# Optimization experiments

Measured on AMD Instinct MI355X. Metric: run time of the kernel, lower is better.

The kernel has to match this reference:

```python
import jax, jax.numpy as jnp
import numpy as np

B, S, H = 1, 2048, 2048
NH, NKV, HD = 16, 4, 128
LAT, RD = 512, 64
ND = HD - RD  # nope_dim = 64
EPS = 1e-6


def _rms(x, g):
    return x * jax.lax.rsqrt(jnp.mean(x * x, axis=-1, keepdims=True) + EPS) * g


def _rotate_half(x):
    x1, x2 = jnp.split(x, 2, axis=-1)
    return jnp.concatenate([-x2, x1], axis=-1)


def _rope(x, cos, sin):
    # x: [B,S,nh,RD]; cos/sin: [S,RD] -> broadcast over batch and heads
    c = cos[None, :, None, :]
    s = sin[None, :, None, :]
    return x * c + _rotate_half(x) * s


def setup_inputs() -> dict:
    key = jax.random.key(0)
    ks = jax.random.split(key, 10)
    x = jax.random.normal(ks[0], (B, S, H), jnp.float32)
    # rotary tables (theta=10000) for rope_dim
    inv = 1.0 / (10000.0 ** (np.arange(0, RD, 2, dtype=np.float32) / RD))
    t = np.arange(S, dtype=np.float32)
    freqs = np.outer(t, inv)  # [S, RD/2]
    emb = np.concatenate([freqs, freqs], axis=-1)  # [S, RD]
    cos = jnp.asarray(np.cos(emb), jnp.float32)
    sin = jnp.asarray(np.sin(emb), jnp.float32)
    sc = lambda fan_in: 1.0 / np.sqrt(fan_in)
    Wq_nope = jax.random.normal(ks[1], (NH * ND, H), jnp.float32) * sc(H)
    Wq_rope = jax.random.normal(ks[2], (NH * RD, H), jnp.float32) * sc(H)
    W_kv_down = jax.random.normal(ks[3], (LAT, H), jnp.float32) * sc(H)
    W_k_nope = jax.random.normal(ks[4], (NKV * ND, LAT), jnp.float32) * sc(LAT)
    W_k_rope = jax.random.normal(ks[5], (NKV * RD, LAT), jnp.float32) * sc(LAT)
    W_v = jax.random.normal(ks[6], (NKV * HD, LAT), jnp.float32) * sc(LAT)
    W_o = jax.random.normal(ks[7], (H, NH * HD), jnp.float32) * sc(NH * HD)
    return {
        "x": x, "cos": cos, "sin": sin,
        "Wq_nope": Wq_nope, "Wq_rope": Wq_rope,
        "g_qnope": jnp.ones((ND,), jnp.float32),
        "g_qrope": jnp.ones((RD,), jnp.float32),
        "W_kv_down": W_kv_down, "g_ckv": jnp.ones((LAT,), jnp.float32),
        "W_k_nope": W_k_nope, "W_k_rope": W_k_rope,
        "W_v": W_v, "W_o": W_o,
    }


def reference(x, cos, sin, Wq_nope, Wq_rope, g_qnope, g_qrope,
              W_kv_down, g_ckv, W_k_nope, W_k_rope, W_v, W_o):
    n_rep = NH // NKV
    # queries: decoupled nope / rope parts, RMSNorm each, RoPE on rope part
    q_nope = _rms((x @ Wq_nope.T).reshape(B, S, NH, ND), g_qnope)
    q_rope = _rms((x @ Wq_rope.T).reshape(B, S, NH, RD), g_qrope)
    q_rope = _rope(q_rope, cos[:S, :RD], sin[:S, :RD])
    q = jnp.concatenate([q_nope, q_rope], axis=-1)  # [B,S,NH,HD]
    # latent KV compression
    c_kv = _rms(x @ W_kv_down.T, g_ckv)  # [B,S,LAT]
    k_nope = (c_kv @ W_k_nope.T).reshape(B, S, NKV, ND)
    k_rope = _rope((c_kv @ W_k_rope.T).reshape(B, S, NKV, RD), cos[:S, :RD], sin[:S, :RD])
    v = (c_kv @ W_v.T).reshape(B, S, NKV, HD)
    k = jnp.concatenate([k_nope, k_rope], axis=-1)  # [B,S,NKV,HD]
    # repeat kv heads
    k = jnp.repeat(k, n_rep, axis=2)  # [B,S,NH,HD]
    v = jnp.repeat(v, n_rep, axis=2)
    # causal attention, softmax in fp32
    scores = jnp.einsum("bqhd,bkhd->bhqk", q, k) / jnp.sqrt(jnp.asarray(HD, jnp.float32))
    causal = jnp.tril(jnp.ones((S, S), bool))
    scores = jnp.where(causal[None, None], scores, -jnp.inf)
    attn = jax.nn.softmax(scores.astype(jnp.float32), axis=-1).astype(q.dtype)
    out = jnp.einsum("bhqk,bkhd->bqhd", attn, v).reshape(B, S, NH * HD)
    return out @ W_o.T  # [B,S,H]
```

## Files before the change

### kernel.cpp

```cpp
#include <hip/hip_runtime.h>
#include <hip/hip_bf16.h>
#include <math.h>

#define TPB 256

typedef __attribute__((ext_vector_type(8))) short bf16x8;
typedef __attribute__((ext_vector_type(4))) float f32x4;

__device__ __forceinline__ short f2bs(float x) {
  __hip_bfloat16 h = __float2bfloat16(x);
  return *reinterpret_cast<short*>(&h);
}

__device__ __forceinline__ void gll16(const void* g, void* l) {
  __builtin_amdgcn_global_load_lds(
      (const __attribute__((address_space(1))) unsigned int*)g,
      (__attribute__((address_space(3))) unsigned int*)l, 16, 0, 0);
}

__global__ __launch_bounds__(TPB) void cvt_f2b(
    const float* __restrict__ s, short* __restrict__ d, int n)
{
  int i = (blockIdx.x * TPB + threadIdx.x) << 2;
  if (i >= n) return;
  const float4 v = *(const float4*)(s + i);
  short4 o;
  o.x = f2bs(v.x); o.y = f2bs(v.y); o.z = f2bs(v.z); o.w = f2bs(v.w);
  *(short4*)(d + i) = o;
}

__global__ __launch_bounds__(TPB) void cvt_weights(
    const float* __restrict__ w0, const float* __restrict__ w1,
    const float* __restrict__ w2, const float* __restrict__ w3,
    const float* __restrict__ w4, const float* __restrict__ w5,
    const float* __restrict__ w6,
    short* __restrict__ Wcat, short* __restrict__ Wkvb, short* __restrict__ Wob)
{
  int b = blockIdx.x;
  const float* src; short* dst; int base;
  if (b < 2048)      { src = w0; dst = Wcat;           base = b; }
  else if (b < 4096) { src = w1; dst = Wcat + 2097152; base = b - 2048; }
  else if (b < 5120) { src = w2; dst = Wcat + 4194304; base = b - 4096; }
  else if (b < 5248) { src = w3; dst = Wkvb;           base = b - 5120; }
  else if (b < 5376) { src = w4; dst = Wkvb + 131072;  base = b - 5248; }
  else if (b < 5632) { src = w5; dst = Wkvb + 262144;  base = b - 5376; }
  else               { src = w6; dst = Wob;            base = b - 5632; }
  int i = base * 1024 + threadIdx.x * 4;
  float4 v = *(const float4*)(src + i);
  short4 o;
  o.x = f2bs(v.x); o.y = f2bs(v.y); o.z = f2bs(v.z); o.w = f2bs(v.w);
  *(short4*)(dst + i) = o;
}

__global__ __launch_bounds__(TPB) void rms512b(
    const float* __restrict__ src, short* __restrict__ dst,
    const float* __restrict__ g, int nrows)
{
  int row = blockIdx.x * (TPB / 64) + (threadIdx.x >> 6);
  int l = threadIdx.x & 63;
  if (row >= nrows) return;
  const float* p = src + (size_t)row * 512;
  float x[8];
  float ss = 0.f;
#pragma unroll
  for (int i = 0; i < 8; ++i) { x[i] = p[i * 64 + l]; ss += x[i] * x[i]; }
#pragma unroll
  for (int msk = 1; msk < 64; msk <<= 1) ss += __shfl_xor(ss, msk);
  float r = rsqrtf(ss * (1.0f / 512.0f) + 1e-6f);
#pragma unroll
  for (int i = 0; i < 8; ++i)
    dst[(size_t)row * 512 + i * 64 + l] = f2bs(x[i] * r * g[i * 64 + l]);
}

template <int MODE>
__global__ __launch_bounds__(TPB) void gemm_fused(
    const short* __restrict__ A, const short* __restrict__ W,
    float* __restrict__ Cf, short* __restrict__ qk_out, short* __restrict__ vt,
    float* __restrict__ ckv_f,
    const float* __restrict__ cosb, const float* __restrict__ sinb,
    const float* __restrict__ g_qnope, const float* __restrict__ g_qrope,
    int M, int N, int K, int ldc)
{
  __shared__ short As[2][128 * 64];
  __shared__ short Bs[2][128 * 64];
  const int t = threadIdx.x;
  const int lane = t & 63, wave = t >> 6;
  const int wr = wave >> 1, wc = wave & 1;
  const int li = lane & 15, lh = lane >> 4;
  const int bm = blockIdx.y * 128, bn = blockIdx.x * 128;

  f32x4 acc[4][4];
#pragma unroll
  for (int m = 0; m < 4; ++m)
#pragma unroll
    for (int n = 0; n < 4; ++n) acc[m][n] = (f32x4){0.f, 0.f, 0.f, 0.f};

#define GSTAGE(buf, k0)                                                        \
  {                                                                            \
    _Pragma("unroll") for (int i = 0; i < 4; ++i) {                            \
      int id = i * 256 + t;                                                    \
      int r = id >> 3, cl = id & 7;                                            \
      gll16(A + (size_t)(bm + r) * K + (k0) + ((cl ^ (r & 7)) << 3),           \
            &As[buf][id * 8]);                                                 \
    }                                                                          \
    _Pragma("unroll") for (int i = 0; i < 4; ++i) {                            \
      int id = i * 256 + t;                                                    \
      int r = id >> 3, cl = id & 7;                                            \
      gll16(W + (size_t)(bn + r) * K + (k0) + ((cl ^ (r & 7)) << 3),           \
            &Bs[buf][id * 8]);                                                 \
    }                                                                          \
  }

  GSTAGE(0, 0);
  int cur = 0;
  for (int k0 = 0; k0 < K; k0 += 64) {
    __syncthreads();
    if (k0 + 64 < K) GSTAGE(cur ^ 1, k0 + 64);
    bf16x8 af[2][4], bf[2][4];
#pragma unroll
    for (int m = 0; m < 4; ++m) {
      int r = wr * 64 + m * 16 + li;
#pragma unroll
      for (int kd = 0; kd < 2; ++kd)
        af[kd][m] = *(const bf16x8*)&As[cur][r * 64 + (((kd * 4 + lh) ^ (r & 7)) << 3)];
    }
#pragma unroll
    for (int n = 0; n < 4; ++n) {
      int r = wc * 64 + n * 16 + li;
#pragma unroll
      for (int kd = 0; kd < 2; ++kd)
        bf[kd][n] = *(const bf16x8*)&Bs[cur][r * 64 + (((kd * 4 + lh) ^ (r & 7)) << 3)];
    }
#pragma unroll
    for (int kd = 0; kd < 2; ++kd)
#pragma unroll
      for (int m = 0; m < 4; ++m)
#pragma unroll
        for (int n = 0; n < 4; ++n)
          acc[m][n] = __builtin_amdgcn_mfma_f32_16x16x32_bf16(af[kd][m], bf[kd][n],
                                                              acc[m][n], 0, 0, 0);
    cur ^= 1;
  }
#undef GSTAGE

  const int colbase = bn + wc * 64;

  if (MODE == 0) {
#pragma unroll
    for (int m = 0; m < 4; ++m) {
      int gm = bm + wr * 64 + m * 16 + lh * 4;
#pragma unroll
      for (int n = 0; n < 4; ++n) {
        int gn = colbase + n * 16 + li;
#pragma unroll
        for (int j = 0; j < 4; ++j)
          Cf[(size_t)(gm + j) * ldc + gn] = acc[m][n][j];
      }
    }
  }

  if (MODE == 1) {
    if (colbase < 2048) {
      const bool isrope = colbase >= 1024;
      const int head = (colbase & 1023) >> 6;
      const float* g = isrope ? g_qrope : g_qnope;
      float gv[4];
#pragma unroll
      for (int nf = 0; nf < 4; ++nf) gv[nf] = g[nf * 16 + li];
#pragma unroll
      for (int m = 0; m < 4; ++m) {
#pragma unroll
        for (int j = 0; j < 4; ++j) {
          int s = bm + wr * 64 + m * 16 + lh * 4 + j;
          float sum = acc[m][0][j] * acc[m][0][j] + acc[m][1][j] * acc[m][1][j] +
                      acc[m][2][j] * acc[m][2][j] + acc[m][3][j] * acc[m][3][j];
          sum += __shfl_xor(sum, 1); sum += __shfl_xor(sum, 2);
          sum += __shfl_xor(sum, 4); sum += __shfl_xor(sum, 8);
          float r = rsqrtf(sum * (1.0f / 64.0f) + 1e-6f);
          float y[4];
#pragma unroll
          for (int nf = 0; nf < 4; ++nf) y[nf] = acc[m][nf][j] * r * gv[nf];
          if (isrope) {
            float yr[4];
#pragma unroll
            for (int nf = 0; nf < 4; ++nf) {
              int c = nf * 16 + li;
              float cs = cosb[s * 64 + c], sn = sinb[s * 64 + c];
              float par = (nf < 2) ? -y[nf + 2] : y[nf - 2];
              yr[nf] = y[nf] * cs + par * sn;
            }
#pragma unroll
            for (int nf = 0; nf < 4; ++nf) y[nf] = yr[nf];
          }
#pragma unroll
          for (int nf = 0; nf < 4; ++nf)
            qk_out[(size_t)s * 2048 + head * 128 + (isrope ? 64 : 0) + nf * 16 + li] =
                f2bs(y[nf]);
        }
      }
    } else {
      const int c0 = colbase - 2048;
#pragma unroll
      for (int m = 0; m < 4; ++m) {
        int gm = bm + wr * 64 + m * 16 + lh * 4;
#pragma unroll
        for (int n = 0; n < 4; ++n) {
          int c = c0 + n * 16 + li;
#pragma unroll
          for (int j = 0; j < 4; ++j)
            ckv_f[(size_t)(gm + j) * 512 + c] = acc[m][n][j];
        }
      }
    }
  }

  if (MODE == 2) {
    if (colbase < 512) {
      const bool isrope = colbase >= 256;
      const int kvh = (colbase & 255) >> 6;
#pragma unroll
      for (int m = 0; m < 4; ++m) {
#pragma unroll
        for (int j = 0; j < 4; ++j) {
          int s = bm + wr * 64 + m * 16 + lh * 4 + j;
          float y[4];
#pragma unroll
          for (int nf = 0; nf < 4; ++nf) y[nf] = acc[m][nf][j];
          if (isrope) {
            float yr[4];
#pragma unroll
            for (int nf = 0; nf < 4; ++nf) {
              int c = nf * 16 + li;
              float cs = cosb[s * 64 + c], sn = sinb[s * 64 + c];
              float par = (nf < 2) ? -y[nf + 2] : y[nf - 2];
              yr[nf] = y[nf] * cs + par * sn;
            }
#pragma unroll
            for (int nf = 0; nf < 4; ++nf) y[nf] = yr[nf];
          }
#pragma unroll
          for (int nf = 0; nf < 4; ++nf)
            qk_out[(size_t)s * 512 + kvh * 128 + (isrope ? 64 : 0) + nf * 16 + li] =
                f2bs(y[nf]);
        }
      }
    } else {
#pragma unroll
      for (int m = 0; m < 4; ++m) {
        int s0 = bm + wr * 64 + m * 16 + lh * 4;
#pragma unroll
        for (int nf = 0; nf < 4; ++nf) {
          int d = colbase - 512 + nf * 16 + li;
          int kvh = d >> 7, dd = d & 127;
          short4 pk;
          pk.x = f2bs(acc[m][nf][0]); pk.y = f2bs(acc[m][nf][1]);
          pk.z = f2bs(acc[m][nf][2]); pk.w = f2bs(acc[m][nf][3]);
          *(short4*)&vt[(size_t)kvh * 262144 + (size_t)dd * 2048 + s0] = pk;
        }
      }
    }
  }
}

__global__ __launch_bounds__(TPB) void attn_mfma(
    const short* __restrict__ qb, const short* __restrict__ kb,
    const short* __restrict__ vt, short* __restrict__ ob)
{
  __shared__ short Ks[2][64 * 128];
  __shared__ short Vs[2][128 * 64];
  __shared__ short Ps[4][16 * 64];
  const int h = blockIdx.x;
  const int qt = gridDim.y - 1 - blockIdx.y;
  const int kvh = h >> 2;
  const int t = threadIdx.x, lane = t & 63, wave = t >> 6;
  const int li = lane & 15, lh = lane >> 4;
  const int q0 = qt * 64, q0w = q0 + wave * 16;
  const float scale = 0.08838834764831845f;

  bf16x8 qf[4];
#pragma unroll
  for (int kd = 0; kd < 4; ++kd)
    qf[kd] = *(const bf16x8*)(qb + (size_t)(q0w + li) * 2048 + h * 128 + kd * 32 + lh * 8);

  f32x4 o[8];
#pragma unroll
  for (int n = 0; n < 8; ++n) o[n] = (f32x4){0.f, 0.f, 0.f, 0.f};
  float m_i[4] = {-1e30f, -1e30f, -1e30f, -1e30f};
  float l_i[4] = {0.f, 0.f, 0.f, 0.f};

#define ASTAGE(buf, kbase)                                                     \
  {                                                                            \
    _Pragma("unroll") for (int i = 0; i < 4; ++i) {                            \
      int c = t + i * 256;                                                     \
      int kpos = c >> 4, dcl = (c & 15) ^ (kpos & 7);                          \
      gll16(kb + (size_t)((kbase) + kpos) * 512 + kvh * 128 + dcl * 8,         \
            &Ks[buf][c * 8]);                                                  \
    }                                                                          \
    _Pragma("unroll") for (int i = 0; i < 4; ++i) {                            \
      int c = t + i * 256;                                                     \
      int d = c >> 3, kpl = (c & 7) ^ (d & 7);                                 \
      gll16(vt + (size_t)kvh * 262144 + (size_t)d * 2048 + (kbase) + kpl * 8,  \
            &Vs[buf][c * 8]);                                                  \
    }                                                                          \
  }

  short* pw = Ps[wave];
  const int nkt = qt + 1;
  ASTAGE(0, 0);
  int cur = 0;
  for (int kt = 0; kt < nkt; ++kt) {
    const int kbase = kt * 64;
    __syncthreads();
    if (kt + 1 < nkt) ASTAGE(cur ^ 1, kbase + 64);

    f32x4 s[4];
#pragma unroll
    for (int n = 0; n < 4; ++n) s[n] = (f32x4){0.f, 0.f, 0.f, 0.f};
#pragma unroll
    for (int n = 0; n < 4; ++n) {
      int kpos = n * 16 + li;
#pragma unroll
      for (int kd = 0; kd < 4; ++kd) {
        int cph = (kd * 4 + lh) ^ (kpos & 7);
        bf16x8 kf = *(const bf16x8*)&Ks[cur][kpos * 128 + cph * 8];
        s[n] = __builtin_amdgcn_mfma_f32_16x16x32_bf16(qf[kd], kf, s[n], 0, 0, 0);
      }
    }
    float sv[4][4];
    const bool diag = (kt == nkt - 1);
#pragma unroll
    for (int n = 0; n < 4; ++n)
#pragma unroll
      for (int j = 0; j < 4; ++j) {
        float val = s[n][j] * scale;
        if (diag) {
          int kg = kbase + n * 16 + li;
          int qg = q0w + lh * 4 + j;
          if (kg > qg) val = -1e30f;
        }
        sv[n][j] = val;
      }
    float c_[4];
#pragma unroll
    for (int j = 0; j < 4; ++j) {
      float rm = fmaxf(fmaxf(sv[0][j], sv[1][j]), fmaxf(sv[2][j], sv[3][j]));
      rm = fmaxf(rm, __shfl_xor(rm, 1));
      rm = fmaxf(rm, __shfl_xor(rm, 2));
      rm = fmaxf(rm, __shfl_xor(rm, 4));
      rm = fmaxf(rm, __shfl_xor(rm, 8));
      float mn = fmaxf(m_i[j], rm);
      c_[j] = __expf(m_i[j] - mn);
      m_i[j] = mn;
    }
#pragma unroll
    for (int n = 0; n < 4; ++n)
#pragma unroll
      for (int j = 0; j < 4; ++j) sv[n][j] = __expf(sv[n][j] - m_i[j]);
#pragma unroll
    for (int j = 0; j < 4; ++j) {
      float rs = sv[0][j] + sv[1][j] + sv[2][j] + sv[3][j];
      rs += __shfl_xor(rs, 1);
      rs += __shfl_xor(rs, 2);
      rs += __shfl_xor(rs, 4);
      rs += __shfl_xor(rs, 8);
      l_i[j] = l_i[j] * c_[j] + rs;
    }
#pragma unroll
    for (int n = 0; n < 4; ++n)
#pragma unroll
      for (int j = 0; j < 4; ++j) {
        int qq = lh * 4 + j, kp = n * 16 + li;
        pw[qq * 64 + (kp ^ ((qq & 7) << 3))] = f2bs(sv[n][j]);
      }
#pragma unroll
    for (int n = 0; n < 8; ++n)
#pragma unroll
      for (int j = 0; j < 4; ++j) o[n][j] *= c_[j];
    asm volatile("s_waitcnt lgkmcnt(0)" ::: "memory");
    __builtin_amdgcn_sched_barrier(0);
#pragma unroll
    for (int kk = 0; kk < 2; ++kk) {
      int kp0 = kk * 32 + lh * 8;
      bf16x8 pf = *(const bf16x8*)&pw[li * 64 + (kp0 ^ ((li & 7) << 3))];
#pragma unroll
      for (int n = 0; n < 8; ++n) {
        int d = n * 16 + li;
        bf16x8 vf = *(const bf16x8*)&Vs[cur][d * 64 + (kp0 ^ ((d & 7) << 3))];
        o[n] = __builtin_amdgcn_mfma_f32_16x16x32_bf16(pf, vf, o[n], 0, 0, 0);
      }
    }
    cur ^= 1;
  }
#undef ASTAGE
  float inv[4];
#pragma unroll
  for (int j = 0; j < 4; ++j) inv[j] = 1.0f / l_i[j];
#pragma unroll
  for (int n = 0; n < 8; ++n)
#pragma unroll
    for (int j = 0; j < 4; ++j)
      ob[(size_t)(q0w + lh * 4 + j) * 2048 + h * 128 + n * 16 + li] =
          f2bs(o[n][j] * inv[j]);
}

extern "C" void kernel_launch(void* const* d_in, const int* in_sizes, int n_in,
                              void* d_out, int out_size, void* d_ws, size_t ws_size,
                              hipStream_t stream) {
  const float* x         = (const float*)d_in[0];
  const float* cosb      = (const float*)d_in[1];
  const float* sinb      = (const float*)d_in[2];
  const float* Wq_nope   = (const float*)d_in[3];
  const float* Wq_rope   = (const float*)d_in[4];
  const float* g_qnope   = (const float*)d_in[5];
  const float* g_qrope   = (const float*)d_in[6];
  const float* W_kv_down = (const float*)d_in[7];
  const float* g_ckv     = (const float*)d_in[8];
  const float* W_k_nope  = (const float*)d_in[9];
  const float* W_k_rope  = (const float*)d_in[10];
  const float* W_v       = (const float*)d_in[11];
  const float* W_o       = (const float*)d_in[12];
  float* out = (float*)d_out;

  float* ws = (float*)d_ws;
  float* ckv_f = ws;
  short* sb   = (short*)(ws + 1048576);
  short* xb   = sb;
  short* Wcat = sb + 4194304;
  short* Wkvb = Wcat + 5242880;
  short* Wob  = Wkvb + 524288;
  short* qb   = Wob + 4194304;
  short* ckvb = qb + 4194304;
  short* kb   = ckvb + 1048576;
  short* vt   = kb + 1048576;
  short* aob  = xb;

  dim3 blk(TPB);

  cvt_f2b<<<4096, blk, 0, stream>>>(x, xb, 4194304);
  cvt_weights<<<9728, blk, 0, stream>>>(Wq_nope, Wq_rope, W_kv_down, W_k_nope,
                                        W_k_rope, W_v, W_o, Wcat, Wkvb, Wob);

  gemm_fused<1><<<dim3(20, 16), blk, 0, stream>>>(
      xb, Wcat, nullptr, qb, nullptr, ckv_f, cosb, sinb, g_qnope, g_qrope,
      2048, 2560, 2048, 0);

  rms512b<<<512, blk, 0, stream>>>(ckv_f, ckvb, g_ckv, 2048);

  gemm_fused<2><<<dim3(8, 16), blk, 0, stream>>>(
      ckvb, Wkvb, nullptr, kb, vt, nullptr, cosb, sinb, nullptr, nullptr,
      2048, 1024, 512, 0);

  attn_mfma<<<dim3(16, 32), blk, 0, stream>>>(qb, kb, vt, aob);

  gemm_fused<0><<<dim3(16, 16), blk, 0, stream>>>(
      aob, Wob, out, nullptr, nullptr, nullptr, nullptr, nullptr, nullptr, nullptr,
      2048, 2048, 2048, 2048);
}
```

Measured before the change: 286.2 us.

## Load attention K/V directly from global, tighten GEMM pipeline waits, use exp2 softmax

The attention kernel drops its LDS double-buffering of K and V. Each wave now reads its K and V fragments straight from global memory, which removes block-wide barriers and frees LDS for higher occupancy, at the cost of repeated global and L2 traffic across waves. The softmax folds log2(e) into the scale and uses exp2f, and it skips rescaling the output accumulator when no row maximum changed. The GEMM loop replaces __syncthreads with an explicit lgkmcnt wait plus barrier and a partial vmcnt wait so the next stage's loads can stay in flight, and it raises wave priority around the MFMA block.

```diff
diff --git a/kernel.cpp b/kernel.cpp
--- a/kernel.cpp
+++ b/kernel.cpp
@@ -114,8 +114,17 @@
   GSTAGE(0, 0);
   int cur = 0;
   for (int k0 = 0; k0 < K; k0 += 64) {
-    __syncthreads();
-    if (k0 + 64 < K) GSTAGE(cur ^ 1, k0 + 64);
+    __builtin_amdgcn_sched_barrier(0);
+    asm volatile("s_waitcnt lgkmcnt(0)" ::: "memory");
+    __builtin_amdgcn_s_barrier();
+    __builtin_amdgcn_sched_barrier(0);
+    if (k0 + 64 < K) {
+      GSTAGE(cur ^ 1, k0 + 64);
+      asm volatile("s_waitcnt vmcnt(8)" ::: "memory");
+    } else {
+      asm volatile("s_waitcnt vmcnt(0)" ::: "memory");
+    }
+    __builtin_amdgcn_sched_barrier(0);
     bf16x8 af[2][4], bf[2][4];
 #pragma unroll
     for (int m = 0; m < 4; ++m) {
@@ -131,6 +140,7 @@
       for (int kd = 0; kd < 2; ++kd)
         bf[kd][n] = *(const bf16x8*)&Bs[cur][r * 64 + (((kd * 4 + lh) ^ (r & 7)) << 3)];
     }
+    __builtin_amdgcn_s_setprio(1);
 #pragma unroll
     for (int kd = 0; kd < 2; ++kd)
 #pragma unroll
@@ -139,6 +149,8 @@
         for (int n = 0; n < 4; ++n)
           acc[m][n] = __builtin_amdgcn_mfma_f32_16x16x32_bf16(af[kd][m], bf[kd][n],
                                                               acc[m][n], 0, 0, 0);
+    __builtin_amdgcn_s_setprio(0);
+    __builtin_amdgcn_sched_barrier(0);
     cur ^= 1;
   }
 #undef GSTAGE
@@ -266,16 +278,14 @@
     const short* __restrict__ qb, const short* __restrict__ kb,
     const short* __restrict__ vt, short* __restrict__ ob)
 {
-  __shared__ short Ks[2][64 * 128];
-  __shared__ short Vs[2][128 * 64];
   __shared__ short Ps[4][16 * 64];
   const int h = blockIdx.x;
   const int qt = gridDim.y - 1 - blockIdx.y;
   const int kvh = h >> 2;
   const int t = threadIdx.x, lane = t & 63, wave = t >> 6;
   const int li = lane & 15, lh = lane >> 4;
-  const int q0 = qt * 64, q0w = q0 + wave * 16;
-  const float scale = 0.08838834764831845f;
+  const int q0w = qt * 64 + wave * 16;
+  const float sc2 = 0.08838834764831845f * 1.44269504088896f;
 
   bf16x8 qf[4];
 #pragma unroll
@@ -288,52 +298,35 @@
   float m_i[4] = {-1e30f, -1e30f, -1e30f, -1e30f};
   float l_i[4] = {0.f, 0.f, 0.f, 0.f};
 
-#define ASTAGE(buf, kbase)                                                     \
-  {                                                                            \
-    _Pragma("unroll") for (int i = 0; i < 4; ++i) {                            \
-      int c = t + i * 256;                                                     \
-      int kpos = c >> 4, dcl = (c & 15) ^ (kpos & 7);                          \
-      gll16(kb + (size_t)((kbase) + kpos) * 512 + kvh * 128 + dcl * 8,         \
-            &Ks[buf][c * 8]);                                                  \
-    }                                                                          \
-    _Pragma("unroll") for (int i = 0; i < 4; ++i) {                            \
-      int c = t + i * 256;                                                     \
-      int d = c >> 3, kpl = (c & 7) ^ (d & 7);                                 \
-      gll16(vt + (size_t)kvh * 262144 + (size_t)d * 2048 + (kbase) + kpl * 8,  \
-            &Vs[buf][c * 8]);                                                  \
-    }                                                                          \
-  }
-
   short* pw = Ps[wave];
+  const short* kbh = kb + kvh * 128;
+  const short* vth = vt + (size_t)kvh * 262144;
   const int nkt = qt + 1;
-  ASTAGE(0, 0);
-  int cur = 0;
+
   for (int kt = 0; kt < nkt; ++kt) {
     const int kbase = kt * 64;
-    __syncthreads();
-    if (kt + 1 < nkt) ASTAGE(cur ^ 1, kbase + 64);
-
     f32x4 s[4];
 #pragma unroll
     for (int n = 0; n < 4; ++n) s[n] = (f32x4){0.f, 0.f, 0.f, 0.f};
 #pragma unroll
-    for (int n = 0; n < 4; ++n) {
-      int kpos = n * 16 + li;
-#pragma unroll
-      for (int kd = 0; kd < 4; ++kd) {
-        int cph = (kd * 4 + lh) ^ (kpos & 7);
-        bf16x8 kf = *(const bf16x8*)&Ks[cur][kpos * 128 + cph * 8];
-        s[n] = __builtin_amdgcn_mfma_f32_16x16x32_bf16(qf[kd], kf, s[n], 0, 0, 0);
-      }
+    for (int kd = 0; kd < 4; ++kd) {
+      bf16x8 kf[4];
+#pragma unroll
+      for (int n = 0; n < 4; ++n)
+        kf[n] = *(const bf16x8*)(kbh + (size_t)(kbase + n * 16 + li) * 512 +
+                                 kd * 32 + lh * 8);
+#pragma unroll
+      for (int n = 0; n < 4; ++n)
+        s[n] = __builtin_amdgcn_mfma_f32_16x16x32_bf16(qf[kd], kf[n], s[n], 0, 0, 0);
     }
     float sv[4][4];
-    const bool diag = (kt == nkt - 1);
+    const bool dg = (kt == nkt - 1);
 #pragma unroll
     for (int n = 0; n < 4; ++n)
 #pragma unroll
       for (int j = 0; j < 4; ++j) {
-        float val = s[n][j] * scale;
-        if (diag) {
+        float val = s[n][j] * sc2;
+        if (dg) {
           int kg = kbase + n * 16 + li;
           int qg = q0w + lh * 4 + j;
           if (kg > qg) val = -1e30f;
@@ -341,6 +334,7 @@
         sv[n][j] = val;
       }
     float c_[4];
+    float cmin = 1.f;
 #pragma unroll
     for (int j = 0; j < 4; ++j) {
       float rm = fmaxf(fmaxf(sv[0][j], sv[1][j]), fmaxf(sv[2][j], sv[3][j]));
@@ -349,13 +343,14 @@
       rm = fmaxf(rm, __shfl_xor(rm, 4));
       rm = fmaxf(rm, __shfl_xor(rm, 8));
       float mn = fmaxf(m_i[j], rm);
-      c_[j] = __expf(m_i[j] - mn);
+      c_[j] = exp2f(m_i[j] - mn);
       m_i[j] = mn;
+      cmin = fminf(cmin, c_[j]);
     }
 #pragma unroll
     for (int n = 0; n < 4; ++n)
 #pragma unroll
-      for (int j = 0; j < 4; ++j) sv[n][j] = __expf(sv[n][j] - m_i[j]);
+      for (int j = 0; j < 4; ++j) sv[n][j] = exp2f(sv[n][j] - m_i[j]);
 #pragma unroll
     for (int j = 0; j < 4; ++j) {
       float rs = sv[0][j] + sv[1][j] + sv[2][j] + sv[3][j];
@@ -372,10 +367,12 @@
         int qq = lh * 4 + j, kp = n * 16 + li;
         pw[qq * 64 + (kp ^ ((qq & 7) << 3))] = f2bs(sv[n][j]);
       }
-#pragma unroll
-    for (int n = 0; n < 8; ++n)
-#pragma unroll
-      for (int j = 0; j < 4; ++j) o[n][j] *= c_[j];
+    if (__any(cmin < 1.f)) {
+#pragma unroll
+      for (int n = 0; n < 8; ++n)
+#pragma unroll
+        for (int j = 0; j < 4; ++j) o[n][j] *= c_[j];
+    }
     asm volatile("s_waitcnt lgkmcnt(0)" ::: "memory");
     __builtin_amdgcn_sched_barrier(0);
 #pragma unroll
@@ -384,14 +381,11 @@
       bf16x8 pf = *(const bf16x8*)&pw[li * 64 + (kp0 ^ ((li & 7) << 3))];
 #pragma unroll
       for (int n = 0; n < 8; ++n) {
-        int d = n * 16 + li;
-        bf16x8 vf = *(const bf16x8*)&Vs[cur][d * 64 + (kp0 ^ ((d & 7) << 3))];
+        bf16x8 vf = *(const bf16x8*)(vth + (size_t)(n * 16 + li) * 2048 + kbase + kp0);
         o[n] = __builtin_amdgcn_mfma_f32_16x16x32_bf16(pf, vf, o[n], 0, 0, 0);
       }
     }
-    cur ^= 1;
-  }
-#undef ASTAGE
+  }
   float inv[4];
 #pragma unroll
   for (int j = 0; j < 4; ++j) inv[j] = 1.0f / l_i[j];
```

Result: slower. 394.7 us (+37.9%).
